# Kernel tuning notes

Measured on AMD Instinct MI355X. Metric: run time of the kernel, lower is better.

Reference implementation:

```python
import jax, jax.numpy as jnp
import numpy as np
import math

B, S, D, H = 4, 2048, 1024, 16
DH = D // H  # dim per head = 64


def setup_inputs() -> dict:
    key = jax.random.key(0)
    ks = jax.random.split(key, 12)
    scale = 0.02
    inp = {
        "query": jax.random.normal(ks[0], (B, S, D), jnp.float32),
        "key": jax.random.normal(ks[1], (B, S, D), jnp.float32),
        "value": jax.random.normal(ks[2], (B, S, D), jnp.float32),
        "mask": jnp.zeros((B, S), jnp.float32),  # additive mask, 0 = attend
        "Wq": jax.random.normal(ks[3], (D, D), jnp.float32) * scale,
        "bq": jnp.zeros((D,), jnp.float32),
        "Wk": jax.random.normal(ks[4], (D, D), jnp.float32) * scale,
        "bk": jnp.zeros((D,), jnp.float32),
        "Wv": jax.random.normal(ks[5], (D, D), jnp.float32) * scale,
        "bv": jnp.zeros((D,), jnp.float32),
        "Wo": jax.random.normal(ks[6], (D, D), jnp.float32) * scale,
        "bo": jnp.zeros((D,), jnp.float32),
    }
    return inp


def reference(query, key, value, mask, Wq, bq, Wk, bk, Wv, bv, Wo, bo):
    # Linear projections (torch Linear: x @ W.T + b; here W stored as (in, out))
    def shape(x):  # (B,S,D) -> (B,H,S,DH)
        return x.reshape(B, S, H, DH).transpose(0, 2, 1, 3)

    q = shape(query @ Wq + bq) / math.sqrt(DH)
    k = shape(key @ Wk + bk)
    v = shape(value @ Wv + bv)

    # scores: (B,H,S,S)
    scores = jnp.einsum("bhqd,bhkd->bhqk", q, k)
    scores = scores + mask[:, None, None, :]  # additive mask broadcast
    weights = jax.nn.softmax(scores, axis=-1)
    # dropout omitted (eval mode / p effectively 0 for reference)
    context = jnp.einsum("bhqk,bhkd->bhqd", weights, v)
    context = context.transpose(0, 2, 1, 3).reshape(B, S, D)
    out = context @ Wo + bo
    return out
```

## Files before the change

### kernel.cpp

```cpp
#include <hip/hip_runtime.h>
#include <hip/hip_bf16.h>

#define B_  4
#define S_  2048
#define D_  1024
#define H_  16
#define DH_ 64
#define M_  (B_*S_)

typedef __attribute__((ext_vector_type(8)))  short    bf16x8;
typedef __attribute__((ext_vector_type(4)))  float    f32x4;
typedef __attribute__((ext_vector_type(16))) float    f32x16;
typedef __attribute__((ext_vector_type(2)))  unsigned u32x2;

#define LOG2E 1.4426950408889634f

__device__ __forceinline__ void g2l16(const void* g, void* l) {
    __builtin_amdgcn_global_load_lds(
        (const __attribute__((address_space(1))) unsigned*)g,
        (__attribute__((address_space(3))) unsigned*)l, 16, 0, 0);
}

__global__ __launch_bounds__(256) void wtrans4(
    const float* __restrict__ W0, const float* __restrict__ W1,
    const float* __restrict__ W2, const float* __restrict__ W3,
    __hip_bfloat16* __restrict__ T0, __hip_bfloat16* __restrict__ T1,
    __hip_bfloat16* __restrict__ T2, __hip_bfloat16* __restrict__ T3)
{
    const float* W = blockIdx.z == 0 ? W0 : (blockIdx.z == 1 ? W1 : (blockIdx.z == 2 ? W2 : W3));
    __hip_bfloat16* Wt = blockIdx.z == 0 ? T0 : (blockIdx.z == 1 ? T1 : (blockIdx.z == 2 ? T2 : T3));
    __shared__ float t[32][33];
    const int bx = blockIdx.x * 32;
    const int by = blockIdx.y * 32;
    const int tx = threadIdx.x, ty = threadIdx.y;
    #pragma unroll
    for (int i = 0; i < 32; i += 8)
        t[ty + i][tx] = W[(size_t)(by + ty + i) * D_ + bx + tx];
    __syncthreads();
    #pragma unroll
    for (int i = 0; i < 32; i += 8)
        Wt[(size_t)(bx + ty + i) * D_ + by + tx] = __float2bfloat16(t[tx][ty + i]);
}

__global__ __launch_bounds__(256, 2) void gemm_qkv(
    const float* __restrict__ Xq, const float* __restrict__ Xk, const float* __restrict__ Xv,
    const __hip_bfloat16* __restrict__ WtQ, const __hip_bfloat16* __restrict__ WtK,
    const __hip_bfloat16* __restrict__ WtV,
    const float* __restrict__ bq, const float* __restrict__ bk, const float* __restrict__ bv,
    __hip_bfloat16* __restrict__ Yq, __hip_bfloat16* __restrict__ Yk,
    __hip_bfloat16* __restrict__ Yv)
{
    __shared__ char Af[32768];
    __shared__ char Bb[16384];

    const int flat = blockIdx.x;
    const int xcd  = flat & 7;
    const int t    = flat >> 3;
    const int bz   = t >> 6;
    const int r    = t & 63;
    const int m0   = (xcd * 8 + (r >> 3)) * 128;
    const int n0   = (r & 7) * 128;

    const float* X = bz == 0 ? Xq : (bz == 1 ? Xk : Xv);
    const __hip_bfloat16* Wt = bz == 0 ? WtQ : (bz == 1 ? WtK : WtV);
    const float* bias = bz == 0 ? bq : (bz == 1 ? bk : bv);
    __hip_bfloat16* Y = bz == 0 ? Yq : (bz == 1 ? Yk : Yv);
    const float scale = bz == 0 ? 0.125f * LOG2E : 1.0f;

    const int tid = threadIdx.x;
    const int w = tid >> 6, l = tid & 63;
    const int wm = w >> 1, wn = w & 1;
    const int li = l & 15, lg = l >> 4;

    f32x4 acc[4][4];
    #pragma unroll
    for (int a = 0; a < 4; ++a)
        #pragma unroll
        for (int b = 0; b < 4; ++b)
            acc[a][b] = (f32x4){0.f, 0.f, 0.f, 0.f};

    for (int k0 = 0; k0 < D_; k0 += 64) {
        #pragma unroll
        for (int p = 0; p < 8; ++p) {
            int sl = p * 256 + tid;
            int row = sl >> 4, s = sl & 15;
            int sw = s ^ (row & 15);
            g2l16(X + (size_t)(m0 + row) * D_ + k0 + sw * 4, Af + sl * 16);
        }
        #pragma unroll
        for (int p = 0; p < 4; ++p) {
            int sl = p * 256 + tid;
            int row = sl >> 3, s = sl & 7;
            g2l16(Wt + (size_t)(n0 + row) * D_ + k0 + s * 8, Bb + sl * 16);
        }
        asm volatile("s_waitcnt vmcnt(0)");
        __syncthreads();

        #pragma unroll
        for (int kh = 0; kh < 2; ++kh) {
            bf16x8 af[4], bfr[4];
            #pragma unroll
            for (int mt = 0; mt < 4; ++mt) {
                int row = wm * 64 + mt * 16 + li;
                int bs = kh * 8 + lg * 2;
                f32x4 r0 = *(const f32x4*)(Af + row * 256 + ((bs ^ li) * 16));
                f32x4 r1 = *(const f32x4*)(Af + row * 256 + (((bs + 1) ^ li) * 16));
                union { unsigned u[4]; bf16x8 v; } pk;
                asm("v_cvt_pk_bf16_f32 %0, %1, %2" : "=v"(pk.u[0]) : "v"(r0[0]), "v"(r0[1]));
                asm("v_cvt_pk_bf16_f32 %0, %1, %2" : "=v"(pk.u[1]) : "v"(r0[2]), "v"(r0[3]));
                asm("v_cvt_pk_bf16_f32 %0, %1, %2" : "=v"(pk.u[2]) : "v"(r1[0]), "v"(r1[1]));
                asm("v_cvt_pk_bf16_f32 %0, %1, %2" : "=v"(pk.u[3]) : "v"(r1[2]), "v"(r1[3]));
                af[mt] = pk.v;
            }
            #pragma unroll
            for (int nt = 0; nt < 4; ++nt)
                bfr[nt] = *(const bf16x8*)(Bb + (wn * 64 + nt * 16 + li) * 128 + kh * 64 + lg * 16);
            #pragma unroll
            for (int mt = 0; mt < 4; ++mt)
                #pragma unroll
                for (int nt = 0; nt < 4; ++nt)
                    acc[mt][nt] = __builtin_amdgcn_mfma_f32_16x16x32_bf16(
                        af[mt], bfr[nt], acc[mt][nt], 0, 0, 0);
        }
        __syncthreads();
    }

    #pragma unroll
    for (int mt = 0; mt < 4; ++mt) {
        #pragma unroll
        for (int nt = 0; nt < 4; ++nt) {
            int col = n0 + wn * 64 + nt * 16 + li;
            float bv_ = bias[col];
            #pragma unroll
            for (int i = 0; i < 4; ++i) {
                int row = m0 + wm * 64 + mt * 16 + lg * 4 + i;
                float v = (acc[mt][nt][i] + bv_) * scale;
                if (bz == 2) {
                    int b = row >> 11, s = row & (S_ - 1);
                    int h = col >> 6,  dh = col & 63;
                    Y[((((size_t)b * H_ + h) * DH_ + dh) << 11) + s] = __float2bfloat16(v);
                } else {
                    Y[(size_t)row * D_ + col] = __float2bfloat16(v);
                }
            }
        }
    }
}

__global__ __launch_bounds__(256, 2) void gemm_out(
    const __hip_bfloat16* __restrict__ X, const __hip_bfloat16* __restrict__ Wt,
    const float* __restrict__ bias, float* __restrict__ Y)
{
    __shared__ char Ab[16384];
    __shared__ char Bb[16384];

    const int flat = blockIdx.x;
    const int xcd  = flat & 7;
    const int t    = flat >> 3;
    const int m0   = (xcd * 8 + (t >> 3)) * 128;
    const int n0   = (t & 7) * 128;

    const int tid = threadIdx.x;
    const int w = tid >> 6, l = tid & 63;
    const int wm = w >> 1, wn = w & 1;
    const int li = l & 15, lg = l >> 4;

    f32x4 acc[4][4];
    #pragma unroll
    for (int a = 0; a < 4; ++a)
        #pragma unroll
        for (int b = 0; b < 4; ++b)
            acc[a][b] = (f32x4){0.f, 0.f, 0.f, 0.f};

    for (int k0 = 0; k0 < D_; k0 += 64) {
        #pragma unroll
        for (int p = 0; p < 4; ++p) {
            int sl = p * 256 + tid;
            int row = sl >> 3, s = sl & 7;
            g2l16(X  + (size_t)(m0 + row) * D_ + k0 + s * 8, Ab + sl * 16);
            g2l16(Wt + (size_t)(n0 + row) * D_ + k0 + s * 8, Bb + sl * 16);
        }
        asm volatile("s_waitcnt vmcnt(0)");
        __syncthreads();

        #pragma unroll
        for (int kh = 0; kh < 2; ++kh) {
            bf16x8 af[4], bfr[4];
            #pragma unroll
            for (int mt = 0; mt < 4; ++mt)
                af[mt] = *(const bf16x8*)(Ab + (wm * 64 + mt * 16 + li) * 128 + kh * 64 + lg * 16);
            #pragma unroll
            for (int nt = 0; nt < 4; ++nt)
                bfr[nt] = *(const bf16x8*)(Bb + (wn * 64 + nt * 16 + li) * 128 + kh * 64 + lg * 16);
            #pragma unroll
            for (int mt = 0; mt < 4; ++mt)
                #pragma unroll
                for (int nt = 0; nt < 4; ++nt)
                    acc[mt][nt] = __builtin_amdgcn_mfma_f32_16x16x32_bf16(
                        af[mt], bfr[nt], acc[mt][nt], 0, 0, 0);
        }
        __syncthreads();
    }

    #pragma unroll
    for (int mt = 0; mt < 4; ++mt) {
        #pragma unroll
        for (int nt = 0; nt < 4; ++nt) {
            int col = n0 + wn * 64 + nt * 16 + li;
            float bv_ = bias[col];
            #pragma unroll
            for (int i = 0; i < 4; ++i) {
                int row = m0 + wm * 64 + mt * 16 + lg * 4 + i;
                Y[(size_t)row * D_ + col] = acc[mt][nt][i] + bv_;
            }
        }
    }
}

__global__ __launch_bounds__(256, 4) void attn_mfma(
    const __hip_bfloat16* __restrict__ q, const __hip_bfloat16* __restrict__ k,
    const __hip_bfloat16* __restrict__ vt, const float* __restrict__ mask,
    __hip_bfloat16* __restrict__ ctx)
{
    __shared__ char Kb[2][8192];
    __shared__ char Vb[2][8192];
    __shared__ float mlds[S_];

    const int tid = threadIdx.x;
    const int w = tid >> 6, l = tid & 63;
    const int q31 = l & 31, hi = l >> 5;

    const int bid = blockIdx.x;
    const int j = bid >> 3;
    const int bh = (bid & 7) * 8 + (j >> 4);
    const int q0 = (j & 15) * 128;
    const int bb = bh >> 4, hh = bh & 15;

    const __hip_bfloat16* kbase = k  + (size_t)bb * S_ * D_ + hh * 64;
    const __hip_bfloat16* vbase = vt + (size_t)bh * (DH_ * S_);

    for (int i = tid; i < S_ / 4; i += 256) {
        float4 mv = ((const float4*)(mask + (size_t)bb * S_))[i];
        mv.x *= LOG2E; mv.y *= LOG2E; mv.z *= LOG2E; mv.w *= LOG2E;
        ((float4*)mlds)[i] = mv;
    }

    const int qrow = q0 + w * 32 + q31;
    const __hip_bfloat16* qp = q + (size_t)(bb * S_ + qrow) * D_ + hh * 64;
    bf16x8 qf[4];
    #pragma unroll
    for (int mf = 0; mf < 4; ++mf)
        qf[mf] = *(const bf16x8*)(qp + mf * 16 + hi * 8);

    f32x16 ot0, ot1;
    #pragma unroll
    for (int r = 0; r < 16; ++r) { ot0[r] = 0.f; ot1[r] = 0.f; }
    float lsum = 0.f;

    #pragma unroll
    for (int c = 0; c < 2; ++c) {
        int sl = c * 256 + tid, row = sl >> 3, s = sl & 7, sw = s ^ (row & 7);
        g2l16(kbase + (size_t)row * D_ + sw * 8, Kb[0] + sl * 16);
        g2l16(vbase + (size_t)row * S_ + sw * 8, Vb[0] + sl * 16);
    }
    asm volatile("s_waitcnt vmcnt(0)");
    __syncthreads();

    int cur = 0;
    for (int kt = 0; kt < S_; kt += 64) {
        if (kt + 64 < S_) {
            #pragma unroll
            for (int c = 0; c < 2; ++c) {
                int sl = c * 256 + tid, row = sl >> 3, s = sl & 7, sw = s ^ (row & 7);
                g2l16(kbase + (size_t)(kt + 64 + row) * D_ + sw * 8, Kb[cur ^ 1] + sl * 16);
                g2l16(vbase + (size_t)row * S_ + (kt + 64) + sw * 8, Vb[cur ^ 1] + sl * 16);
            }
        }

        #pragma unroll
        for (int ks = 0; ks < 2; ++ks) {
            f32x16 sc;
            #pragma unroll
            for (int g = 0; g < 4; ++g) {
                f32x4 mq = *(const f32x4*)(mlds + kt + ks * 32 + g * 8 + hi * 4);
                sc[g * 4 + 0] = mq[0]; sc[g * 4 + 1] = mq[1];
                sc[g * 4 + 2] = mq[2]; sc[g * 4 + 3] = mq[3];
            }
            const int arow = ks * 32 + q31;
            __builtin_amdgcn_s_setprio(1);
            #pragma unroll
            for (int mf = 0; mf < 4; ++mf) {
                int slot = (mf * 2 + hi) ^ (arow & 7);
                bf16x8 kf = *(const bf16x8*)(Kb[cur] + arow * 128 + slot * 16);
                sc = __builtin_amdgcn_mfma_f32_32x32x16_bf16(kf, qf[mf], sc, 0, 0, 0);
            }
            __builtin_amdgcn_s_setprio(0);
            float ps[4] = {0.f, 0.f, 0.f, 0.f};
            #pragma unroll
            for (int r = 0; r < 16; ++r) {
                float e = __builtin_amdgcn_exp2f(sc[r]);
                sc[r] = e;
                ps[r & 3] += e;
            }
            lsum += (ps[0] + ps[1]) + (ps[2] + ps[3]);

            unsigned pw[8];
            #pragma unroll
            for (int m = 0; m < 8; ++m) {
                float lo = sc[2 * m], hp = sc[2 * m + 1];
                unsigned r_;
                asm("v_cvt_pk_bf16_f32 %0, %1, %2" : "=v"(r_) : "v"(lo), "v"(hp));
                pw[m] = r_;
            }
            u32x2 s02 = __builtin_amdgcn_permlane32_swap(pw[0], pw[2], false, false);
            u32x2 s13 = __builtin_amdgcn_permlane32_swap(pw[1], pw[3], false, false);
            u32x2 s46 = __builtin_amdgcn_permlane32_swap(pw[4], pw[6], false, false);
            u32x2 s57 = __builtin_amdgcn_permlane32_swap(pw[5], pw[7], false, false);
            union { unsigned u[4]; bf16x8 v; } pf0, pf1;
            pf0.u[0] = s02[0]; pf0.u[1] = s13[0]; pf0.u[2] = s02[1]; pf0.u[3] = s13[1];
            pf1.u[0] = s46[0]; pf1.u[1] = s57[0]; pf1.u[2] = s46[1]; pf1.u[3] = s57[1];

            __builtin_amdgcn_s_setprio(1);
            #pragma unroll
            for (int kh = 0; kh < 2; ++kh) {
                bf16x8 pf = kh ? pf1.v : pf0.v;
                #pragma unroll
                for (int dt = 0; dt < 2; ++dt) {
                    int row = dt * 32 + q31;
                    int slot = (ks * 4 + kh * 2 + hi) ^ (row & 7);
                    bf16x8 vf = *(const bf16x8*)(Vb[cur] + row * 128 + slot * 16);
                    if (dt == 0)
                        ot0 = __builtin_amdgcn_mfma_f32_32x32x16_bf16(vf, pf, ot0, 0, 0, 0);
                    else
                        ot1 = __builtin_amdgcn_mfma_f32_32x32x16_bf16(vf, pf, ot1, 0, 0, 0);
                }
            }
            __builtin_amdgcn_s_setprio(0);
        }
        asm volatile("s_waitcnt vmcnt(0)");
        __syncthreads();
        cur ^= 1;
    }

    float lt = lsum + __shfl_xor(lsum, 32);
    float inv = 1.0f / lt;
    __hip_bfloat16* cp = ctx + (size_t)(bb * S_ + qrow) * D_ + hh * 64;
    #pragma unroll
    for (int dt = 0; dt < 2; ++dt) {
        #pragma unroll
        for (int g = 0; g < 4; ++g) {
            float v0 = (dt ? ot1[g * 4 + 0] : ot0[g * 4 + 0]) * inv;
            float v1 = (dt ? ot1[g * 4 + 1] : ot0[g * 4 + 1]) * inv;
            float v2 = (dt ? ot1[g * 4 + 2] : ot0[g * 4 + 2]) * inv;
            float v3 = (dt ? ot1[g * 4 + 3] : ot0[g * 4 + 3]) * inv;
            unsigned w0, w1;
            asm("v_cvt_pk_bf16_f32 %0, %1, %2" : "=v"(w0) : "v"(v0), "v"(v1));
            asm("v_cvt_pk_bf16_f32 %0, %1, %2" : "=v"(w1) : "v"(v2), "v"(v3));
            u32x2 st; st[0] = w0; st[1] = w1;
            *(u32x2*)(cp + dt * 32 + g * 8 + hi * 4) = st;
        }
    }
}

extern "C" void kernel_launch(void* const* d_in, const int* in_sizes, int n_in,
                              void* d_out, int out_size, void* d_ws, size_t ws_size,
                              hipStream_t stream) {
    const float* query = (const float*)d_in[0];
    const float* key_  = (const float*)d_in[1];
    const float* value = (const float*)d_in[2];
    const float* mask  = (const float*)d_in[3];
    const float* Wq = (const float*)d_in[4];
    const float* bq = (const float*)d_in[5];
    const float* Wk = (const float*)d_in[6];
    const float* bk = (const float*)d_in[7];
    const float* Wv = (const float*)d_in[8];
    const float* bv = (const float*)d_in[9];
    const float* Wo = (const float*)d_in[10];
    const float* bo = (const float*)d_in[11];
    float* out = (float*)d_out;

    const size_t WSZ = (size_t)D_ * D_;
    const size_t ASZ = (size_t)M_ * D_;
    __hip_bfloat16* p   = (__hip_bfloat16*)d_ws;
    __hip_bfloat16* WtQ = p;            p += WSZ;
    __hip_bfloat16* WtK = p;            p += WSZ;
    __hip_bfloat16* WtV = p;            p += WSZ;
    __hip_bfloat16* WtO = p;            p += WSZ;
    __hip_bfloat16* qb  = p;            p += ASZ;
    __hip_bfloat16* kb  = p;            p += ASZ;
    __hip_bfloat16* vtb = p;            p += ASZ;
    __hip_bfloat16* cb  = p;            p += ASZ;

    wtrans4<<<dim3(32, 32, 4), dim3(32, 8), 0, stream>>>(Wq, Wk, Wv, Wo, WtQ, WtK, WtV, WtO);

    gemm_qkv<<<dim3(1536), 256, 0, stream>>>(
        query, key_, value, WtQ, WtK, WtV, bq, bk, bv, qb, kb, vtb);

    attn_mfma<<<dim3((S_ / 128) * B_ * H_), 256, 0, stream>>>(qb, kb, vtb, mask, cb);

    gemm_out<<<dim3(512), 256, 0, stream>>>(cb, WtO, bo, out);
}
```

Before: 205.4 us.

## Double-buffer QKV projection GEMM with K-step 32 and async prefetch

The QKV projection GEMM now keeps two LDS buffers. The next K-slice (32 wide) is issued with global_load_lds before the MFMAs on the current slice run, so global loads overlap with compute instead of serialising load, wait, then compute. Total LDS per block stays at 48KB. The price is twice as many barriers and waits per K, each iteration doing half as much MFMA work as before, and a swizzle changed to fit 8 chunks per row. Some unused index variables are left in the code.

```diff
diff --git a/kernel.cpp b/kernel.cpp
--- a/kernel.cpp
+++ b/kernel.cpp
@@ -50,8 +50,8 @@
     __hip_bfloat16* __restrict__ Yq, __hip_bfloat16* __restrict__ Yk,
     __hip_bfloat16* __restrict__ Yv)
 {
-    __shared__ char Af[32768];
-    __shared__ char Bb[16384];
+    __shared__ char Af[2][16384];
+    __shared__ char Bb[2][8192];
 
     const int flat = blockIdx.x;
     const int xcd  = flat & 7;
@@ -72,6 +72,9 @@
     const int wm = w >> 1, wn = w & 1;
     const int li = l & 15, lg = l >> 4;
 
+    const int aRow = tid >> 3, aS = tid & 7;
+    const int bRow = tid >> 2, bS = tid & 3;
+
     f32x4 acc[4][4];
     #pragma unroll
     for (int a = 0; a < 4; ++a)
@@ -79,50 +82,66 @@
         for (int b = 0; b < 4; ++b)
             acc[a][b] = (f32x4){0.f, 0.f, 0.f, 0.f};
 
-    for (int k0 = 0; k0 < D_; k0 += 64) {
-        #pragma unroll
-        for (int p = 0; p < 8; ++p) {
-            int sl = p * 256 + tid;
-            int row = sl >> 4, s = sl & 15;
-            int sw = s ^ (row & 15);
-            g2l16(X + (size_t)(m0 + row) * D_ + k0 + sw * 4, Af + sl * 16);
-        }
-        #pragma unroll
-        for (int p = 0; p < 4; ++p) {
-            int sl = p * 256 + tid;
-            int row = sl >> 3, s = sl & 7;
-            g2l16(Wt + (size_t)(n0 + row) * D_ + k0 + s * 8, Bb + sl * 16);
-        }
+    #pragma unroll
+    for (int p = 0; p < 4; ++p) {
+        int sl = p * 256 + tid;
+        int row = sl >> 3, s = sl & 7, sw = s ^ (row & 7);
+        g2l16(X + (size_t)(m0 + row) * D_ + sw * 4, Af[0] + sl * 16);
+    }
+    #pragma unroll
+    for (int c = 0; c < 2; ++c) {
+        int sl = c * 256 + tid;
+        int row = sl >> 2, s = sl & 3;
+        g2l16(Wt + (size_t)(n0 + row) * D_ + s * 8, Bb[0] + sl * 16);
+    }
+    asm volatile("s_waitcnt vmcnt(0)");
+    __syncthreads();
+
+    int cur = 0;
+    for (int k0 = 0; k0 < D_; k0 += 32) {
+        const int kn = k0 + 32;
+        if (kn < D_) {
+            #pragma unroll
+            for (int p = 0; p < 4; ++p) {
+                int sl = p * 256 + tid;
+                int row = sl >> 3, s = sl & 7, sw = s ^ (row & 7);
+                g2l16(X + (size_t)(m0 + row) * D_ + kn + sw * 4, Af[cur ^ 1] + sl * 16);
+            }
+            #pragma unroll
+            for (int c = 0; c < 2; ++c) {
+                int sl = c * 256 + tid;
+                int row = sl >> 2, s = sl & 3;
+                g2l16(Wt + (size_t)(n0 + row) * D_ + kn + s * 8, Bb[cur ^ 1] + sl * 16);
+            }
+        }
+
+        bf16x8 af[4], bfr[4];
+        #pragma unroll
+        for (int mt = 0; mt < 4; ++mt) {
+            int row = wm * 64 + mt * 16 + li;
+            int bs = lg * 2;
+            f32x4 r0 = *(const f32x4*)(Af[cur] + row * 128 + ((bs ^ (row & 7)) * 16));
+            f32x4 r1 = *(const f32x4*)(Af[cur] + row * 128 + (((bs + 1) ^ (row & 7)) * 16));
+            union { unsigned u[4]; bf16x8 v; } pk;
+            asm("v_cvt_pk_bf16_f32 %0, %1, %2" : "=v"(pk.u[0]) : "v"(r0[0]), "v"(r0[1]));
+            asm("v_cvt_pk_bf16_f32 %0, %1, %2" : "=v"(pk.u[1]) : "v"(r0[2]), "v"(r0[3]));
+            asm("v_cvt_pk_bf16_f32 %0, %1, %2" : "=v"(pk.u[2]) : "v"(r1[0]), "v"(r1[1]));
+            asm("v_cvt_pk_bf16_f32 %0, %1, %2" : "=v"(pk.u[3]) : "v"(r1[2]), "v"(r1[3]));
+            af[mt] = pk.v;
+        }
+        #pragma unroll
+        for (int nt = 0; nt < 4; ++nt)
+            bfr[nt] = *(const bf16x8*)(Bb[cur] + (wn * 64 + nt * 16 + li) * 64 + lg * 16);
+        #pragma unroll
+        for (int mt = 0; mt < 4; ++mt)
+            #pragma unroll
+            for (int nt = 0; nt < 4; ++nt)
+                acc[mt][nt] = __builtin_amdgcn_mfma_f32_16x16x32_bf16(
+                    af[mt], bfr[nt], acc[mt][nt], 0, 0, 0);
+
         asm volatile("s_waitcnt vmcnt(0)");
         __syncthreads();
-
-        #pragma unroll
-        for (int kh = 0; kh < 2; ++kh) {
-            bf16x8 af[4], bfr[4];
-            #pragma unroll
-            for (int mt = 0; mt < 4; ++mt) {
-                int row = wm * 64 + mt * 16 + li;
-                int bs = kh * 8 + lg * 2;
-                f32x4 r0 = *(const f32x4*)(Af + row * 256 + ((bs ^ li) * 16));
-                f32x4 r1 = *(const f32x4*)(Af + row * 256 + (((bs + 1) ^ li) * 16));
-                union { unsigned u[4]; bf16x8 v; } pk;
-                asm("v_cvt_pk_bf16_f32 %0, %1, %2" : "=v"(pk.u[0]) : "v"(r0[0]), "v"(r0[1]));
-                asm("v_cvt_pk_bf16_f32 %0, %1, %2" : "=v"(pk.u[1]) : "v"(r0[2]), "v"(r0[3]));
-                asm("v_cvt_pk_bf16_f32 %0, %1, %2" : "=v"(pk.u[2]) : "v"(r1[0]), "v"(r1[1]));
-                asm("v_cvt_pk_bf16_f32 %0, %1, %2" : "=v"(pk.u[3]) : "v"(r1[2]), "v"(r1[3]));
-                af[mt] = pk.v;
-            }
-            #pragma unroll
-            for (int nt = 0; nt < 4; ++nt)
-                bfr[nt] = *(const bf16x8*)(Bb + (wn * 64 + nt * 16 + li) * 128 + kh * 64 + lg * 16);
-            #pragma unroll
-            for (int mt = 0; mt < 4; ++mt)
-                #pragma unroll
-                for (int nt = 0; nt < 4; ++nt)
-                    acc[mt][nt] = __builtin_amdgcn_mfma_f32_16x16x32_bf16(
-                        af[mt], bfr[nt], acc[mt][nt], 0, 0, 0);
-        }
-        __syncthreads();
+        cur ^= 1;
     }
 
     #pragma unroll
@@ -145,6 +164,7 @@
             }
         }
     }
+    (void)aRow; (void)aS; (void)bRow; (void)bS;
 }
 
 __global__ __launch_bounds__(256, 2) void gemm_out(
```

Result: no change. 208.9 us (+1.7%).
